# Kernel optimization log

Hardware: AMD Instinct MI355X
Metric: run time of the kernel (lower is better)

Reference implementation:

```python
import jax, jax.numpy as jnp
import numpy as np

MARGIN = 1.0

def masked_maximum(data, mask, axis=1):
    axis_min = jnp.min(data, axis=axis, keepdims=True)
    return jnp.max((data - axis_min) * mask, axis=axis, keepdims=True) + axis_min

def masked_minimum(data, mask, axis=1):
    axis_max = jnp.max(data, axis=axis, keepdims=True)
    return jnp.min((data - axis_max) * mask, axis=axis, keepdims=True) + axis_max

def setup_inputs() -> dict:
    key = jax.random.key(0)
    k1, k2 = jax.random.split(key)
    B = 512
    pdist_matrix = jax.random.uniform(k1, (B, B), dtype=jnp.float32)
    target = jax.random.randint(k2, (B,), 0, 64, dtype=jnp.int64)
    return {"pdist_matrix": pdist_matrix, "target": target}

def reference(pdist_matrix, target):
    B = pdist_matrix.shape[0]
    labels = target.astype(jnp.int32)[:, None]                    # [B,1]
    adjacency = labels == labels.T                                # [B,B] bool
    adjacency_not = ~adjacency

    # Tile pdist over anchor-positive pairs: [B*B, B]
    pdist_tile = jnp.tile(pdist_matrix, (B, 1))
    # mask[i*B+j, k] = (label[j] != label[k]) & (d(j,k) > d(j,i))
    mask = jnp.tile(adjacency_not, (B, 1)) & (
        pdist_tile > pdist_matrix.T.reshape(-1, 1))
    mask_final = (jnp.sum(mask.astype(jnp.float32), axis=1, keepdims=True)
                  > 0.0).reshape(B, B).T                          # [B,B]

    adjacency_not_f = adjacency_not.astype(jnp.float32)
    mask_f = mask.astype(jnp.float32)

    negatives_outside = masked_minimum(pdist_tile, mask_f).reshape(B, B).T
    negatives_inside = jnp.tile(
        masked_maximum(pdist_matrix, adjacency_not_f), (1, B))    # [B,B]
    semi_hard_negatives = jnp.where(mask_final, negatives_outside,
                                    negatives_inside)

    loss_mat = MARGIN + pdist_matrix - semi_hard_negatives
    mask_positives = adjacency.astype(jnp.float32) - jnp.eye(B, dtype=jnp.float32)
    num_positives = jnp.maximum(jnp.sum(mask_positives), 1.0)
    triplet_loss = jnp.sum(jnp.maximum(loss_mat * mask_positives, 0.0)) / num_positives
    return triplet_loss
```

## Files before the change

### kernel.cpp

```cpp
#include <hip/hip_runtime.h>
#include <math.h>

#define BB 512
#define NT 256
#define NW 4

__global__ __launch_bounds__(256) void tshl_row_kernel(
    const float* __restrict__ pdist, const int* __restrict__ target,
    float* __restrict__ row_sum, float* __restrict__ row_cnt)
{
    __shared__ float srow[BB];
    __shared__ int   slab[BB];
    __shared__ float swmax[NW], swmin[NW];
    __shared__ int   scnt[2 * NW];
    __shared__ int   spos[BB];
    __shared__ float spart[BB][NW];
    __shared__ float ssum[NW];

    const int j    = blockIdx.x;
    const int t    = threadIdx.x;
    const int w    = t >> 6;
    const int lane = t & 63;

    srow[t]       = pdist[j * BB + t];
    srow[t + 256] = pdist[j * BB + t + 256];
    slab[t]       = target[t];
    slab[t + 256] = target[t + 256];
    __syncthreads();

    const int   myLab = slab[j];
    const float d1 = srow[t], d2 = srow[t + 256];
    const int   l1 = slab[t], l2 = slab[t + 256];
    const bool  n1 = (l1 != myLab), n2 = (l2 != myLab);

    float lmax = -INFINITY;
    float lmin = fminf(d1, d2);
    if (n1) lmax = d1;
    if (n2) lmax = fmaxf(lmax, d2);
    #pragma unroll
    for (int m = 32; m; m >>= 1) {
        lmax = fmaxf(lmax, __shfl_xor(lmax, m));
        lmin = fminf(lmin, __shfl_xor(lmin, m));
    }
    if (lane == 0) { swmax[w] = lmax; swmin[w] = lmin; }

    const bool f1 = (l1 == myLab) && (t != j);
    const bool f2 = (l2 == myLab) && (t + 256 != j);
    const unsigned long long m1 = __ballot(f1);
    const unsigned long long m2 = __ballot(f2);
    if (lane == 0) { scnt[w] = __popcll(m1); scnt[NW + w] = __popcll(m2); }
    __syncthreads();

    int npos = 0;
    int pre[2 * NW];
    #pragma unroll
    for (int e = 0; e < 2 * NW; ++e) { pre[e] = npos; npos += scnt[e]; }
    const unsigned long long lmask = (1ULL << lane) - 1ULL;
    if (f1) spos[pre[w]      + __popcll(m1 & lmask)] = t;
    if (f2) spos[pre[NW + w] + __popcll(m2 & lmask)] = t + 256;

    const float rmaxv = fmaxf(fmaxf(swmax[0], swmax[1]), fmaxf(swmax[2], swmax[3]));
    const float rminv = fminf(fminf(swmin[0], swmin[1]), fminf(swmin[2], swmin[3]));
    const float neg_in = (rmaxv == -INFINITY) ? rminv : rmaxv;
    __syncthreads();

    for (int q = 0; q < npos; ++q) {
        const int   i    = spos[q];
        const float dpos = srow[i];
        float c = INFINITY;
        if (n1 && d1 > dpos) c = d1;
        if (n2 && d2 > dpos) c = fminf(c, d2);
        #pragma unroll
        for (int m = 32; m; m >>= 1) c = fminf(c, __shfl_xor(c, m));
        if (lane == 0) spart[q][w] = c;
    }
    __syncthreads();

    float psum = 0.0f;
    for (int q = t; q < npos; q += NT) {
        const float mv = fminf(fminf(spart[q][0], spart[q][1]),
                               fminf(spart[q][2], spart[q][3]));
        const float dpos = srow[spos[q]];
        const float shn  = (mv < INFINITY) ? mv : neg_in;
        psum += fmaxf(1.0f + dpos - shn, 0.0f);
    }
    #pragma unroll
    for (int m = 32; m; m >>= 1) psum += __shfl_xor(psum, m);
    if (lane == 0) ssum[w] = psum;
    __syncthreads();
    if (t == 0) {
        row_sum[j] = ssum[0] + ssum[1] + ssum[2] + ssum[3];
        row_cnt[j] = (float)npos;
    }
}

__global__ __launch_bounds__(512) void tshl_final_kernel(
    const float* __restrict__ row_sum, const float* __restrict__ row_cnt,
    float* __restrict__ out)
{
    __shared__ float s1[NW * 2], s2[NW * 2];
    const int t = threadIdx.x;
    const int w = t >> 6;
    const int lane = t & 63;
    float a = row_sum[t];
    float b = row_cnt[t];
    #pragma unroll
    for (int m = 32; m; m >>= 1) {
        a += __shfl_xor(a, m);
        b += __shfl_xor(b, m);
    }
    if (lane == 0) { s1[w] = a; s2[w] = b; }
    __syncthreads();
    if (t == 0) {
        float sum = 0.0f, cnt = 0.0f;
        #pragma unroll
        for (int e = 0; e < NW * 2; ++e) { sum += s1[e]; cnt += s2[e]; }
        out[0] = sum / fmaxf(cnt, 1.0f);
    }
}

extern "C" void kernel_launch(void* const* d_in, const int* in_sizes, int n_in,
                              void* d_out, int out_size, void* d_ws, size_t ws_size,
                              hipStream_t stream) {
    const float* pdist  = (const float*)d_in[0];
    const int*   target = (const int*)d_in[1];
    float* ws      = (float*)d_ws;
    float* row_sum = ws;
    float* row_cnt = ws + BB;
    float* out     = (float*)d_out;

    tshl_row_kernel<<<BB, NT, 0, stream>>>(pdist, target, row_sum, row_cnt);
    tshl_final_kernel<<<1, BB, 0, stream>>>(row_sum, row_cnt, out);
}
```

Before: 13.62 us.

## Fuse row and final reduction into single-wave kernel with last-block atomic reduce

Replaces the 256-thread row kernel and separate final kernel with one 64-thread (single wavefront) kernel per row. Each lane holds 8 distances in registers, positives are enumerated via ballot and shuffle instead of shared-memory compaction, and the final mean is computed by whichever block increments an atomic counter last. This removes __syncthreads, the shared-memory staging and the second launch, but serialises the per-positive min over a single wave. The counter is never reset; it relies on wraparound modulo BB.

```diff
diff --git a/kernel.cpp b/kernel.cpp
--- a/kernel.cpp
+++ b/kernel.cpp
@@ -2,120 +2,94 @@
 #include <math.h>
 
 #define BB 512
-#define NT 256
-#define NW 4
 
-__global__ __launch_bounds__(256) void tshl_row_kernel(
+__global__ __launch_bounds__(64) void tshl_kernel(
     const float* __restrict__ pdist, const int* __restrict__ target,
-    float* __restrict__ row_sum, float* __restrict__ row_cnt)
+    float* __restrict__ row_sum, float* __restrict__ row_cnt,
+    unsigned int* __restrict__ counter, float* __restrict__ out)
 {
-    __shared__ float srow[BB];
-    __shared__ int   slab[BB];
-    __shared__ float swmax[NW], swmin[NW];
-    __shared__ int   scnt[2 * NW];
-    __shared__ int   spos[BB];
-    __shared__ float spart[BB][NW];
-    __shared__ float ssum[NW];
+    const int j    = blockIdx.x;
+    const int lane = threadIdx.x;
 
-    const int j    = blockIdx.x;
-    const int t    = threadIdx.x;
-    const int w    = t >> 6;
-    const int lane = t & 63;
+    const int myLab = target[j];
 
-    srow[t]       = pdist[j * BB + t];
-    srow[t + 256] = pdist[j * BB + t + 256];
-    slab[t]       = target[t];
-    slab[t + 256] = target[t + 256];
-    __syncthreads();
+    float d[8];
+    int   lab[8];
+    #pragma unroll
+    for (int u = 0; u < 8; ++u) {
+        const int c = lane + 64 * u;
+        d[u]   = pdist[j * BB + c];
+        lab[u] = target[c];
+    }
 
-    const int   myLab = slab[j];
-    const float d1 = srow[t], d2 = srow[t + 256];
-    const int   l1 = slab[t], l2 = slab[t + 256];
-    const bool  n1 = (l1 != myLab), n2 = (l2 != myLab);
-
-    float lmax = -INFINITY;
-    float lmin = fminf(d1, d2);
-    if (n1) lmax = d1;
-    if (n2) lmax = fmaxf(lmax, d2);
+    bool neg[8], pos[8];
+    float lmax = -INFINITY, lmin = INFINITY;
+    #pragma unroll
+    for (int u = 0; u < 8; ++u) {
+        neg[u] = (lab[u] != myLab);
+        pos[u] = (!neg[u]) && (lane + 64 * u != j);
+        lmin = fminf(lmin, d[u]);
+        if (neg[u]) lmax = fmaxf(lmax, d[u]);
+    }
     #pragma unroll
     for (int m = 32; m; m >>= 1) {
         lmax = fmaxf(lmax, __shfl_xor(lmax, m));
         lmin = fminf(lmin, __shfl_xor(lmin, m));
     }
-    if (lane == 0) { swmax[w] = lmax; swmin[w] = lmin; }
-
-    const bool f1 = (l1 == myLab) && (t != j);
-    const bool f2 = (l2 == myLab) && (t + 256 != j);
-    const unsigned long long m1 = __ballot(f1);
-    const unsigned long long m2 = __ballot(f2);
-    if (lane == 0) { scnt[w] = __popcll(m1); scnt[NW + w] = __popcll(m2); }
-    __syncthreads();
-
-    int npos = 0;
-    int pre[2 * NW];
-    #pragma unroll
-    for (int e = 0; e < 2 * NW; ++e) { pre[e] = npos; npos += scnt[e]; }
-    const unsigned long long lmask = (1ULL << lane) - 1ULL;
-    if (f1) spos[pre[w]      + __popcll(m1 & lmask)] = t;
-    if (f2) spos[pre[NW + w] + __popcll(m2 & lmask)] = t + 256;
-
-    const float rmaxv = fmaxf(fmaxf(swmax[0], swmax[1]), fmaxf(swmax[2], swmax[3]));
-    const float rminv = fminf(fminf(swmin[0], swmin[1]), fminf(swmin[2], swmin[3]));
-    const float neg_in = (rmaxv == -INFINITY) ? rminv : rmaxv;
-    __syncthreads();
-
-    for (int q = 0; q < npos; ++q) {
-        const int   i    = spos[q];
-        const float dpos = srow[i];
-        float c = INFINITY;
-        if (n1 && d1 > dpos) c = d1;
-        if (n2 && d2 > dpos) c = fminf(c, d2);
-        #pragma unroll
-        for (int m = 32; m; m >>= 1) c = fminf(c, __shfl_xor(c, m));
-        if (lane == 0) spart[q][w] = c;
-    }
-    __syncthreads();
+    const float neg_in = (lmax == -INFINITY) ? lmin : lmax;
 
     float psum = 0.0f;
-    for (int q = t; q < npos; q += NT) {
-        const float mv = fminf(fminf(spart[q][0], spart[q][1]),
-                               fminf(spart[q][2], spart[q][3]));
-        const float dpos = srow[spos[q]];
-        const float shn  = (mv < INFINITY) ? mv : neg_in;
-        psum += fmaxf(1.0f + dpos - shn, 0.0f);
+    int   npos = 0;
+    #pragma unroll
+    for (int u = 0; u < 8; ++u) {
+        unsigned long long bal = __ballot(pos[u]);
+        npos += __popcll(bal);
+        while (bal) {
+            const int src = __builtin_ctzll(bal);
+            bal &= bal - 1;
+            const float dpos = __shfl(d[u], src);
+            float c = INFINITY;
+            #pragma unroll
+            for (int v = 0; v < 8; ++v)
+                if (neg[v] && d[v] > dpos) c = fminf(c, d[v]);
+            #pragma unroll
+            for (int m = 32; m; m >>= 1) c = fminf(c, __shfl_xor(c, m));
+            const float shn = (c < INFINITY) ? c : neg_in;
+            psum += fmaxf(1.0f + dpos - shn, 0.0f);
+        }
     }
-    #pragma unroll
-    for (int m = 32; m; m >>= 1) psum += __shfl_xor(psum, m);
-    if (lane == 0) ssum[w] = psum;
-    __syncthreads();
-    if (t == 0) {
-        row_sum[j] = ssum[0] + ssum[1] + ssum[2] + ssum[3];
-        row_cnt[j] = (float)npos;
+
+    if (lane == 0) {
+        __hip_atomic_store(&row_sum[j], psum, __ATOMIC_RELAXED,
+                           __HIP_MEMORY_SCOPE_AGENT);
+        __hip_atomic_store(&row_cnt[j], (float)npos, __ATOMIC_RELAXED,
+                           __HIP_MEMORY_SCOPE_AGENT);
     }
-}
+    __threadfence();
 
-__global__ __launch_bounds__(512) void tshl_final_kernel(
-    const float* __restrict__ row_sum, const float* __restrict__ row_cnt,
-    float* __restrict__ out)
-{
-    __shared__ float s1[NW * 2], s2[NW * 2];
-    const int t = threadIdx.x;
-    const int w = t >> 6;
-    const int lane = t & 63;
-    float a = row_sum[t];
-    float b = row_cnt[t];
-    #pragma unroll
-    for (int m = 32; m; m >>= 1) {
-        a += __shfl_xor(a, m);
-        b += __shfl_xor(b, m);
-    }
-    if (lane == 0) { s1[w] = a; s2[w] = b; }
-    __syncthreads();
-    if (t == 0) {
-        float sum = 0.0f, cnt = 0.0f;
+    unsigned int old = 0;
+    if (lane == 0)
+        old = __hip_atomic_fetch_add(counter, 1u, __ATOMIC_ACQ_REL,
+                                     __HIP_MEMORY_SCOPE_AGENT);
+    old = __shfl(old, 0);
+
+    if ((old & (BB - 1)) == (BB - 1)) {
+        __threadfence();
+        float s = 0.0f, cn = 0.0f;
         #pragma unroll
-        for (int e = 0; e < NW * 2; ++e) { sum += s1[e]; cnt += s2[e]; }
-        out[0] = sum / fmaxf(cnt, 1.0f);
+        for (int u = 0; u < 8; ++u) {
+            const int r = lane + 64 * u;
+            s  += __hip_atomic_load(&row_sum[r], __ATOMIC_RELAXED,
+                                    __HIP_MEMORY_SCOPE_AGENT);
+            cn += __hip_atomic_load(&row_cnt[r], __ATOMIC_RELAXED,
+                                    __HIP_MEMORY_SCOPE_AGENT);
+        }
+        #pragma unroll
+        for (int m = 32; m; m >>= 1) {
+            s  += __shfl_xor(s, m);
+            cn += __shfl_xor(cn, m);
+        }
+        if (lane == 0) out[0] = s / fmaxf(cn, 1.0f);
     }
 }
 
@@ -124,11 +98,12 @@
                               hipStream_t stream) {
     const float* pdist  = (const float*)d_in[0];
     const int*   target = (const int*)d_in[1];
-    float* ws      = (float*)d_ws;
-    float* row_sum = ws;
-    float* row_cnt = ws + BB;
-    float* out     = (float*)d_out;
+    float* ws           = (float*)d_ws;
+    float* row_sum      = ws;
+    float* row_cnt      = ws + BB;
+    unsigned int* counter = (unsigned int*)(ws + 2 * BB);
+    float* out          = (float*)d_out;
 
-    tshl_row_kernel<<<BB, NT, 0, stream>>>(pdist, target, row_sum, row_cnt);
-    tshl_final_kernel<<<1, BB, 0, stream>>>(row_sum, row_cnt, out);
+    tshl_kernel<<<BB, 64, 0, stream>>>(pdist, target, row_sum, row_cnt,
+                                       counter, out);
 }
```

Measured after the change: 30.21 us. 122% more time.
